# Performance work log

Measured on AMD Instinct MI355X. Metric: run time of the kernel, lower is better.

Reference implementation:

```python
import jax, jax.numpy as jnp
import numpy as np

N, E, IN, ED, HID, B, K = 50000, 800000, 128, 64, 256, 128, 1000


def setup_inputs() -> dict:
    key = jax.random.key(0)
    ks = jax.random.split(key, 16)

    def lin(k, fi, fo):
        k1, k2 = jax.random.split(k)
        s = 1.0 / np.sqrt(fi)
        return (jax.random.uniform(k1, (fi, fo), jnp.float32, -s, s),
                jax.random.uniform(k2, (fo,), jnp.float32, -s, s))

    We, be = lin(ks[0], ED, IN)        # GINEConv edge projection edge_dim -> in_channels
    W1, b1 = lin(ks[1], IN, HID)       # GINE nn layer 1
    W2, b2 = lin(ks[2], HID, HID)      # GINE nn layer 2
    Wg1, bg1 = lin(ks[3], HID, 128)    # gate_nn layer 1
    Wg2, bg2 = lin(ks[4], 128, 1)      # gate_nn layer 2
    Wh, bh = lin(ks[5], HID, K)        # head

    x = jax.random.normal(ks[6], (N, IN), jnp.float32)
    edge_index = jax.random.randint(ks[7], (2, E), 0, N, jnp.int64)
    edge_attr = jax.random.normal(ks[8], (E, ED), jnp.float32)
    batch = jnp.sort(jax.random.randint(ks[9], (N,), 0, B, jnp.int64))

    return {"x": x, "edge_index": edge_index, "edge_attr": edge_attr, "batch": batch,
            "We": We, "be": be, "W1": W1, "b1": b1, "W2": W2, "b2": b2,
            "Wg1": Wg1, "bg1": bg1, "Wg2": Wg2, "bg2": bg2, "Wh": Wh, "bh": bh}


def reference(x, edge_index, edge_attr, batch, We, be, W1, b1, W2, b2,
              Wg1, bg1, Wg2, bg2, Wh, bh):
    src, dst = edge_index[0], edge_index[1]
    # GINEConv message: ReLU(x_j + Lin(edge_attr)), scatter-add to dst (eps=0)
    e = edge_attr @ We + be                      # [E, IN]
    m = jax.nn.relu(x[src] + e)                  # [E, IN]
    agg = jax.ops.segment_sum(m, dst, num_segments=N)  # [N, IN]
    h = x + agg                                  # (1+eps)*x + agg, eps=0
    h = jax.nn.relu(h @ W1 + b1) @ W2 + b2       # [N, HID]
    # GlobalAttention: segment softmax of gate over graphs, weighted sum
    gate = jax.nn.relu(h @ Wg1 + bg1) @ Wg2 + bg2            # [N, 1]
    gmax = jax.ops.segment_max(gate, batch, num_segments=B)  # [B, 1]
    a = jnp.exp(gate - gmax[batch])
    denom = jax.ops.segment_sum(a, batch, num_segments=B)    # [B, 1]
    attn = a / denom[batch]
    pooled = jax.ops.segment_sum(attn * h, batch, num_segments=B)  # [B, HID]
    logits = pooled @ Wh + bh                    # [B, K]
    return (logits, pooled)
```

## Files before the change

### kernel.cpp

```cpp
#include <hip/hip_runtime.h>
#include <stdint.h>

#define NN    50000
#define EE    800000
#define IN_C  128
#define ED_C  64
#define HID_C 256
#define BB    128
#define KK    1000
#define G1_C  128
#define NV    50176


typedef __attribute__((ext_vector_type(8))) short bfrag;
typedef __attribute__((ext_vector_type(4))) float f4acc;

__device__ __forceinline__ unsigned short f2bs(float f){
  unsigned u = __float_as_uint(f);
  return (unsigned short)((u + 0x7fffu + ((u >> 16) & 1u)) >> 16);
}
__device__ __forceinline__ float bs2f(unsigned short s){
  return __uint_as_float(((unsigned)s) << 16);
}

__device__ __forceinline__ void atomicMaxFloat(float* addr, float val){
  int old = __float_as_int(*addr);
  while (__int_as_float(old) < val){
    int assumed = old;
    old = atomicCAS((int*)addr, assumed, __float_as_int(val));
    if (old == assumed) break;
  }
}

__global__ __launch_bounds__(256) void k_prep(
    const float* __restrict__ We, const float* __restrict__ W1,
    const float* __restrict__ W2, const float* __restrict__ Wg1,
    unsigned short* __restrict__ Wet, unsigned short* __restrict__ W1t,
    unsigned short* __restrict__ W2t, unsigned short* __restrict__ Wg1t)
{
  int i = blockIdx.x * 256 + threadIdx.x;
  if (i < 128 * 64){ int c = i >> 6, k = i & 63;  Wet[i]  = f2bs(We[k * 128 + c]); }
  if (i < 256 * 128){ int n = i >> 7, k = i & 127; W1t[i]  = f2bs(W1[k * 256 + n]); }
  if (i < 256 * 256){ int n = i >> 8, k = i & 255; W2t[i]  = f2bs(W2[k * 256 + n]); }
  if (i < 128 * 256){ int n = i >> 8, k = i & 255; Wg1t[i] = f2bs(Wg1[k * 128 + n]); }
}

__global__ __launch_bounds__(256) void k_init(float* __restrict__ agg,
                                              int* __restrict__ cnt,
                                              int* __restrict__ fill,
                                              int* __restrict__ aux,
                                              float* __restrict__ gmax,
                                              float* __restrict__ denom,
                                              float* __restrict__ pooled){
  size_t i = (size_t)blockIdx.x * 256 + threadIdx.x;
  if (i < (size_t)NN * IN_C) agg[i] = 0.f;
  if (i < NV){ cnt[i] = 0; fill[i] = 0; }
  if (i < 256) aux[i] = 0;
  if (i < BB){ gmax[i] = -1e30f; denom[i] = 0.f; }
  if (i < BB * HID_C) pooled[i] = 0.f;
}

__global__ __launch_bounds__(256) void k_hist(const int* __restrict__ ei,
                                              int* __restrict__ cnt){
  int e = blockIdx.x * 256 + threadIdx.x;
  if (e < EE) atomicAdd(&cnt[ei[EE + e]], 1);
}

__global__ __launch_bounds__(256) void k_scan1(const int* __restrict__ cnt,
                                               int* __restrict__ off,
                                               int* __restrict__ aux){
  __shared__ int s[256];
  int t = threadIdx.x, i = blockIdx.x * 256 + t;
  int val = cnt[i];
  s[t] = val; __syncthreads();
#pragma unroll
  for (int o = 1; o < 256; o <<= 1){
    int v = (t >= o) ? s[t - o] : 0;
    __syncthreads();
    s[t] += v;
    __syncthreads();
  }
  off[i] = s[t] - val;
  if (t == 255) aux[blockIdx.x] = s[255];
}

__global__ __launch_bounds__(256) void k_scan2(int* __restrict__ aux){
  __shared__ int s[256];
  int t = threadIdx.x;
  int val = aux[t];
  s[t] = val; __syncthreads();
#pragma unroll
  for (int o = 1; o < 256; o <<= 1){
    int v = (t >= o) ? s[t - o] : 0;
    __syncthreads();
    s[t] += v;
    __syncthreads();
  }
  aux[t] = s[t] - val;
}

__global__ __launch_bounds__(256) void k_scan3(int* __restrict__ off,
                                               const int* __restrict__ aux){
  int i = blockIdx.x * 256 + threadIdx.x;
  off[i] += aux[blockIdx.x];
}

__global__ __launch_bounds__(256) void k_scatter(const int* __restrict__ ei,
                                                 const int* __restrict__ off,
                                                 int* __restrict__ fill,
                                                 uint4* __restrict__ sorted){
  int e = blockIdx.x * 256 + threadIdx.x;
  if (e < EE){
    int s = ei[e], d = ei[EE + e];
    int pos = off[d] + atomicAdd(&fill[d], 1);
    sorted[pos] = make_uint4((unsigned)e, (unsigned)s, (unsigned)d, 0u);
  }
}

__global__ __launch_bounds__(256) void k_edge2(
    const float* __restrict__ x, const uint4* __restrict__ sorted,
    const float* __restrict__ edge_attr,
    const unsigned short* __restrict__ Wet, const float* __restrict__ be,
    float* __restrict__ agg)
{
  __shared__ float msgS[128 * 130];
  __shared__ uint4 sE[128];
  __shared__ float bridgeS[128];
  unsigned short* eaS = (unsigned short*)msgS;

  const int tid = threadIdx.x;
  const int e0 = blockIdx.x * 128;
  if (tid < 128) sE[tid] = sorted[e0 + tid];
  __syncthreads();
#pragma unroll
  for (int t = 0; t < 8; ++t){
    int f4 = t * 256 + tid;
    int er = f4 >> 4;
    int kk = (f4 & 15) * 4;
    int eid = (int)sE[er].x;
    const float4 v = *(const float4*)(edge_attr + (size_t)eid * ED_C + kk);
    unsigned p0 = (unsigned)f2bs(v.x) | ((unsigned)f2bs(v.y) << 16);
    unsigned p1 = (unsigned)f2bs(v.z) | ((unsigned)f2bs(v.w) << 16);
    *(uint2*)&eaS[er * 72 + kk] = make_uint2(p0, p1);
  }
  __syncthreads();

  const int lane = tid & 63, wv = tid >> 6;
  const int q = lane >> 4, l15 = lane & 15;

  f4acc acc[2][8];
  const f4acc zz = {0.f, 0.f, 0.f, 0.f};
#pragma unroll
  for (int mt = 0; mt < 2; ++mt)
#pragma unroll
    for (int nt = 0; nt < 8; ++nt) acc[mt][nt] = zz;

#pragma unroll
  for (int ks = 0; ks < 2; ++ks){
    bfrag a[2], b[8];
#pragma unroll
    for (int mt = 0; mt < 2; ++mt){
      int m = wv * 32 + mt * 16 + l15;
      a[mt] = *(const bfrag*)&eaS[m * 72 + ks * 32 + q * 8];
    }
#pragma unroll
    for (int nt = 0; nt < 8; ++nt){
      int c = nt * 16 + l15;
      b[nt] = *(const bfrag*)(Wet + c * ED_C + ks * 32 + q * 8);
    }
#pragma unroll
    for (int mt = 0; mt < 2; ++mt)
#pragma unroll
      for (int nt = 0; nt < 8; ++nt)
        acc[mt][nt] = __builtin_amdgcn_mfma_f32_16x16x32_bf16(a[mt], b[nt], acc[mt][nt], 0, 0, 0);
  }

  float bev[8];
#pragma unroll
  for (int nt = 0; nt < 8; ++nt) bev[nt] = be[nt * 16 + l15];

  __syncthreads();

#pragma unroll
  for (int mt = 0; mt < 2; ++mt){
    const int g = wv * 32 + mt * 16 + q * 4;
    int sr[4];
#pragma unroll
    for (int r = 0; r < 4; ++r) sr[r] = (int)sE[g + r].y;
#pragma unroll
    for (int nt = 0; nt < 8; ++nt){
      int c = nt * 16 + l15;
#pragma unroll
      for (int r = 0; r < 4; ++r){
        float v = acc[mt][nt][r] + bev[nt] + x[(size_t)sr[r] * IN_C + c];
        v = v > 0.f ? v : 0.f;
        msgS[(g + r) * 130 + c] = v;
      }
    }
  }
  __syncthreads();

  const int col = tid & 127;
  const int h = tid >> 7;
  const int rbeg = h * 64, rend = rbeg + 64;
  const bool bridged = ((int)sE[63].z == (int)sE[64].z);

  int cur = (int)sE[rbeg].z;
  int runstart = rbeg;
  float run = 0.f;
  float firstSum = 0.f; int firstDst = cur;
  bool firstPending = (h == 1);

  for (int r = rbeg; r < rend; ++r){
    int d = (int)sE[r].z;
    if (d != cur){
      if (firstPending){
        firstSum = run; firstDst = cur; firstPending = false;
      } else {
        if (h == 0 && runstart == 0)
          atomicAdd(&agg[(size_t)cur * IN_C + col], run);
        else
          agg[(size_t)cur * IN_C + col] = run;
      }
      run = 0.f; cur = d; runstart = r;
    }
    run += msgS[r * 130 + col];
  }

  if (h == 0){
    if (bridged){
      bridgeS[col] = run;
    } else {
      if (runstart == 0) atomicAdd(&agg[(size_t)cur * IN_C + col], run);
      else               agg[(size_t)cur * IN_C + col] = run;
    }
  }
  __syncthreads();
  if (h == 1){
    if (firstPending){
      float s = run + (bridged ? bridgeS[col] : 0.f);
      atomicAdd(&agg[(size_t)cur * IN_C + col], s);
    } else {
      float s = firstSum + (bridged ? bridgeS[col] : 0.f);
      bool touches0 = bridged && ((int)sE[0].z == firstDst);
      if (touches0) atomicAdd(&agg[(size_t)firstDst * IN_C + col], s);
      else          agg[(size_t)firstDst * IN_C + col] = s;
      atomicAdd(&agg[(size_t)cur * IN_C + col], run);
    }
  }
}

__global__ __launch_bounds__(256) void k_h0(const float* __restrict__ agg,
                                            const float* __restrict__ x,
                                            unsigned short* __restrict__ h0b){
  int i = blockIdx.x * 256 + threadIdx.x;
  if (i < NN * IN_C) h0b[i] = f2bs(agg[i] + x[i]);
}

template<int K, bool RELU, bool OF32, bool OB16>
__global__ __launch_bounds__(256) void k_gemm(
    const unsigned short* __restrict__ A, const unsigned short* __restrict__ Wt,
    const float* __restrict__ bias, float* __restrict__ outf,
    unsigned short* __restrict__ outb, int M, int Ntot)
{
  __shared__ unsigned short aS[64 * 40];
  __shared__ unsigned short bS[128 * 40];
  const int tid = threadIdx.x;
  const int lane = tid & 63, wv = tid >> 6;
  const int wi = wv >> 1, wj = wv & 1;
  const int q = lane >> 4, l15 = lane & 15;
  const int mb0 = blockIdx.x * 64;
  const int nb0 = blockIdx.y * 128;
  const int arow = tid >> 2, achk = tid & 3;

  f4acc acc[2][4];
  const f4acc zz = {0.f, 0.f, 0.f, 0.f};
#pragma unroll
  for (int mt = 0; mt < 2; ++mt)
#pragma unroll
    for (int nt = 0; nt < 4; ++nt) acc[mt][nt] = zz;

  for (int ks = 0; ks < K / 32; ++ks){
    {
      int m = mb0 + arow; if (m >= M) m = M - 1;
      const uint4 v = *(const uint4*)(A + (size_t)m * K + ks * 32 + achk * 8);
      *(uint4*)&aS[arow * 40 + achk * 8] = v;
    }
#pragma unroll
    for (int i = 0; i < 2; ++i){
      int idx = i * 256 + tid;
      int row = idx >> 2, chk = idx & 3;
      const uint4 v = *(const uint4*)(Wt + (size_t)(nb0 + row) * K + ks * 32 + chk * 8);
      *(uint4*)&bS[row * 40 + chk * 8] = v;
    }
    __syncthreads();
    bfrag a[2], b[4];
#pragma unroll
    for (int mt = 0; mt < 2; ++mt)
      a[mt] = *(const bfrag*)&aS[(wi * 32 + mt * 16 + l15) * 40 + q * 8];
#pragma unroll
    for (int nt = 0; nt < 4; ++nt)
      b[nt] = *(const bfrag*)&bS[(wj * 64 + nt * 16 + l15) * 40 + q * 8];
#pragma unroll
    for (int mt = 0; mt < 2; ++mt)
#pragma unroll
      for (int nt = 0; nt < 4; ++nt)
        acc[mt][nt] = __builtin_amdgcn_mfma_f32_16x16x32_bf16(a[mt], b[nt], acc[mt][nt], 0, 0, 0);
    __syncthreads();
  }

  const int mb = mb0 + wi * 32;
  const int nb = nb0 + wj * 64;
#pragma unroll
  for (int nt = 0; nt < 4; ++nt){
    int c = nb + nt * 16 + l15;
    float bv = bias[c];
#pragma unroll
    for (int mt = 0; mt < 2; ++mt){
#pragma unroll
      for (int r = 0; r < 4; ++r){
        int m = mb + mt * 16 + q * 4 + r;
        if (m < M){
          float v = acc[mt][nt][r] + bv;
          if (RELU) v = v > 0.f ? v : 0.f;
          if (OF32) outf[(size_t)m * Ntot + c] = v;
          if (OB16) outb[(size_t)m * Ntot + c] = f2bs(v);
        }
      }
    }
  }
}

__global__ __launch_bounds__(256) void k_gate2(const float* __restrict__ g1,
                                               const float* __restrict__ Wg2,
                                               const float* __restrict__ bg2,
                                               float* __restrict__ gate, int nrows){
  const int lane = threadIdx.x & 63, wv = threadIdx.x >> 6;
  const float2 w2 = *(const float2*)(Wg2 + lane * 2);
  const float bg = bg2[0];
  for (int r = blockIdx.x * 4 + wv; r < nrows; r += gridDim.x * 4){
    const float2 a2 = *(const float2*)(g1 + (size_t)r * G1_C + lane * 2);
    float p = a2.x * w2.x + a2.y * w2.y;
#pragma unroll
    for (int off = 32; off > 0; off >>= 1) p += __shfl_down(p, off);
    if (lane == 0) gate[r] = p + bg;
  }
}

__global__ __launch_bounds__(256) void k_gmax(const float* __restrict__ gate,
                                              const int* __restrict__ batch,
                                              float* __restrict__ gmax, int nrows){
  __shared__ float red[256];
  const int tid = threadIdx.x;
  const int n0 = blockIdx.x * 256;
  const int n = n0 + tid;
  const int nlast = (n0 + 255 < nrows) ? n0 + 255 : nrows - 1;
  const int bmin = batch[n0], bmax = batch[nlast];
  float val = -3e38f; int b = bmax;
  if (n < nrows){ b = batch[n]; val = gate[n]; }
  for (int bb = bmin; bb <= bmax; ++bb){
    red[tid] = (b == bb) ? val : -3e38f;
    __syncthreads();
    for (int s = 128; s > 0; s >>= 1){
      if (tid < s) red[tid] = fmaxf(red[tid], red[tid + s]);
      __syncthreads();
    }
    if (tid == 0 && red[0] > -1e37f) atomicMaxFloat(&gmax[bb], red[0]);
    __syncthreads();
  }
}

__global__ __launch_bounds__(256) void k_expsum(const float* __restrict__ gate,
                                                const int* __restrict__ batch,
                                                const float* __restrict__ gmax,
                                                float* __restrict__ aexp,
                                                float* __restrict__ denom, int nrows){
  __shared__ float red[256];
  const int tid = threadIdx.x;
  const int n0 = blockIdx.x * 256;
  const int n = n0 + tid;
  const int nlast = (n0 + 255 < nrows) ? n0 + 255 : nrows - 1;
  const int bmin = batch[n0], bmax = batch[nlast];
  float val = 0.f; int b = bmax;
  if (n < nrows){
    b = batch[n];
    val = expf(gate[n] - gmax[b]);
    aexp[n] = val;
  }
  for (int bb = bmin; bb <= bmax; ++bb){
    red[tid] = (b == bb) ? val : 0.f;
    __syncthreads();
    for (int s = 128; s > 0; s >>= 1){
      if (tid < s) red[tid] += red[tid + s];
      __syncthreads();
    }
    if (tid == 0 && red[0] != 0.f) atomicAdd(&denom[bb], red[0]);
    __syncthreads();
  }
}

__global__ __launch_bounds__(256) void k_pool(const unsigned short* __restrict__ h2b,
                                              const float* __restrict__ aexp,
                                              const float* __restrict__ denom,
                                              const int* __restrict__ batch,
                                              float* __restrict__ pooled, int nrows){
  const int c = threadIdx.x;
  const int n0 = blockIdx.x * 256;
  int n1 = n0 + 256; if (n1 > nrows) n1 = nrows;
  float acc = 0.f;
  int curb = batch[n0];
  for (int n = n0; n < n1; ++n){
    int b = batch[n];
    if (b != curb){
      atomicAdd(&pooled[(size_t)curb * HID_C + c], acc);
      acc = 0.f; curb = b;
    }
    float wgt = aexp[n] / denom[b];
    acc = fmaf(wgt, bs2f(h2b[(size_t)n * HID_C + c]), acc);
  }
  atomicAdd(&pooled[(size_t)curb * HID_C + c], acc);
}

__global__ __launch_bounds__(256) void k_head(const float* __restrict__ pooled,
                                              const float* __restrict__ Wh,
                                              const float* __restrict__ bh,
                                              float* __restrict__ out_logits,
                                              float* __restrict__ out_pooled){
  __shared__ float p[HID_C];
  const int b = blockIdx.x, t = threadIdx.x;
  float pv = pooled[(size_t)b * HID_C + t];
  p[t] = pv;
  out_pooled[(size_t)b * HID_C + t] = pv;
  __syncthreads();
  for (int c = t; c < KK; c += 256){
    float acc = bh[c];
#pragma unroll 8
    for (int k = 0; k < HID_C; ++k)
      acc = fmaf(p[k], Wh[k * KK + c], acc);
    out_logits[(size_t)b * KK + c] = acc;
  }
}

extern "C" void kernel_launch(void* const* d_in, const int* in_sizes, int n_in,
                              void* d_out, int out_size, void* d_ws, size_t ws_size,
                              hipStream_t stream) {
  const float* x   = (const float*)d_in[0];
  const int*   ei  = (const int*)d_in[1];
  const float* ea  = (const float*)d_in[2];
  const int*   batch = (const int*)d_in[3];
  const float* We  = (const float*)d_in[4];
  const float* be  = (const float*)d_in[5];
  const float* W1  = (const float*)d_in[6];
  const float* b1  = (const float*)d_in[7];
  const float* W2  = (const float*)d_in[8];
  const float* b2  = (const float*)d_in[9];
  const float* Wg1 = (const float*)d_in[10];
  const float* bg1 = (const float*)d_in[11];
  const float* Wg2 = (const float*)d_in[12];
  const float* bg2 = (const float*)d_in[13];
  const float* Wh  = (const float*)d_in[14];
  const float* bh  = (const float*)d_in[15];

  float* out_logits = (float*)d_out;
  float* out_pooled = out_logits + (size_t)BB * KK;

  float* agg    = (float*)d_ws;
  float* gate   = agg   + (size_t)NN * IN_C;
  float* aexp   = gate  + NN;
  float* gmax   = aexp  + NN;
  float* denom  = gmax  + BB;
  float* pooled = denom + BB;
  float* fend   = pooled + (size_t)BB * HID_C;
  unsigned short* h0b  = (unsigned short*)fend;
  unsigned short* h1b  = h0b + (size_t)NN * IN_C;
  unsigned short* h2b  = h1b + (size_t)NN * HID_C;
  unsigned short* Wet  = h2b + (size_t)NN * HID_C;
  unsigned short* W1t  = Wet + 128 * 64;
  unsigned short* W2t  = W1t + 256 * 128;
  unsigned short* Wg1t = W2t + 256 * 256;
  float* g1f = agg;
  uint4* sorted = (uint4*)h1b;
  int* cnt  = (int*)(sorted + EE);
  int* off  = cnt + NV;
  int* fill = off + NV;
  int* aux  = fill + NV;

  k_prep<<<256, 256, 0, stream>>>(We, W1, W2, Wg1, Wet, W1t, W2t, Wg1t);
  k_init<<<(NN * IN_C + 255) / 256, 256, 0, stream>>>(agg, cnt, fill, aux, gmax, denom, pooled);
  k_hist   <<<(EE + 255) / 256, 256, 0, stream>>>(ei, cnt);
  k_scan1  <<<NV / 256, 256, 0, stream>>>(cnt, off, aux);
  k_scan2  <<<1, 256, 0, stream>>>(aux);
  k_scan3  <<<NV / 256, 256, 0, stream>>>(off, aux);
  k_scatter<<<(EE + 255) / 256, 256, 0, stream>>>(ei, off, fill, sorted);
  k_edge2<<<EE / 128, 256, 0, stream>>>(x, sorted, ea, Wet, be, agg);
  k_h0<<<(NN * IN_C + 255) / 256, 256, 0, stream>>>(agg, x, h0b);
  k_gemm<128, true,  false, true ><<<dim3(782, 2), 256, 0, stream>>>(h0b, W1t, b1, (float*)0, h1b, NN, HID_C);
  k_gemm<256, false, false, true ><<<dim3(782, 2), 256, 0, stream>>>(h1b, W2t, b2, (float*)0, h2b, NN, HID_C);
  k_gemm<256, true,  true,  false><<<dim3(782, 1), 256, 0, stream>>>(h2b, Wg1t, bg1, g1f, (unsigned short*)0, NN, G1_C);
  k_gate2<<<3125, 256, 0, stream>>>(g1f, Wg2, bg2, gate, NN);
  k_gmax  <<<(NN + 255) / 256, 256, 0, stream>>>(gate, batch, gmax, NN);
  k_expsum<<<(NN + 255) / 256, 256, 0, stream>>>(gate, batch, gmax, aexp, denom, NN);
  k_pool  <<<(NN + 255) / 256, 256, 0, stream>>>(h2b, aexp, denom, batch, pooled, NN);
  k_head<<<BB, 256, 0, stream>>>(pooled, Wh, bh, out_logits, out_pooled);
}
```

Baseline: 750.5 us.

## Prefetch x rows as float4 and segment-reduce edge messages by precomputed runs

The kernel now issues coalesced float4 loads of each edge's source row of x at kernel start, so the latency overlaps the edge-attr staging and MFMA work. This replaces the per-element scalar gathers that ran after the matmul. Run boundaries of destination nodes are found with a ballot/popcount prefix and stored in shared memory. The two half-blocks then reduce alternating runs, replacing the serial bridged two-half scan. It also pads the shared row stride to 132 and requests two blocks per CU, at the cost of 64 registers per thread for the x prefetch and possible spilling or reduced occupancy.

```diff
diff --git a/kernel.cpp b/kernel.cpp
--- a/kernel.cpp
+++ b/kernel.cpp
@@ -117,21 +117,37 @@
   }
 }
 
-__global__ __launch_bounds__(256) void k_edge2(
+__global__ __launch_bounds__(256, 2) void k_edge2(
     const float* __restrict__ x, const uint4* __restrict__ sorted,
     const float* __restrict__ edge_attr,
     const unsigned short* __restrict__ Wet, const float* __restrict__ be,
     float* __restrict__ agg)
 {
-  __shared__ float msgS[128 * 130];
+  __shared__ float msgS[128 * 132];
   __shared__ uint4 sE[128];
-  __shared__ float bridgeS[128];
+  __shared__ unsigned long long maskS[2];
+  __shared__ int runStart[132];
+  __shared__ int nRunsS;
   unsigned short* eaS = (unsigned short*)msgS;
 
   const int tid = threadIdx.x;
   const int e0 = blockIdx.x * 128;
   if (tid < 128) sE[tid] = sorted[e0 + tid];
   __syncthreads();
+
+  const int xrow = tid >> 1;
+  const int xc0 = (tid & 1) * 64;
+  const float* xptr = x + (size_t)((int)sE[xrow].y) * IN_C + xc0;
+  float4 xr[16];
+#pragma unroll
+  for (int j = 0; j < 16; ++j) xr[j] = *(const float4*)(xptr + j * 4);
+
+  if (tid < 128){
+    bool flag = (tid == 0) || ((int)sE[tid].z != (int)sE[tid - 1].z);
+    unsigned long long m = __ballot(flag);
+    if ((tid & 63) == 0) maskS[tid >> 6] = m;
+  }
+
 #pragma unroll
   for (int t = 0; t < 8; ++t){
     int f4 = t * 256 + tid;
@@ -145,6 +161,18 @@
   }
   __syncthreads();
 
+  if (tid < 128){
+    int lane = tid & 63, wvi = tid >> 6;
+    unsigned long long mw = maskS[wvi];
+    int pre = __popcll(mw & ((1ull << lane) - 1ull)) + (wvi ? __popcll(maskS[0]) : 0);
+    if ((mw >> lane) & 1ull) runStart[pre] = tid;
+    if (tid == 0){
+      int nr = __popcll(maskS[0]) + __popcll(maskS[1]);
+      nRunsS = nr;
+      runStart[nr] = 128;
+    }
+  }
+
   const int lane = tid & 63, wv = tid >> 6;
   const int q = lane >> 4, l15 = lane & 15;
 
@@ -184,68 +212,43 @@
 #pragma unroll
   for (int mt = 0; mt < 2; ++mt){
     const int g = wv * 32 + mt * 16 + q * 4;
-    int sr[4];
-#pragma unroll
-    for (int r = 0; r < 4; ++r) sr[r] = (int)sE[g + r].y;
 #pragma unroll
     for (int nt = 0; nt < 8; ++nt){
       int c = nt * 16 + l15;
 #pragma unroll
-      for (int r = 0; r < 4; ++r){
-        float v = acc[mt][nt][r] + bev[nt] + x[(size_t)sr[r] * IN_C + c];
-        v = v > 0.f ? v : 0.f;
-        msgS[(g + r) * 130 + c] = v;
-      }
+      for (int r = 0; r < 4; ++r)
+        msgS[(g + r) * 132 + c] = acc[mt][nt][r] + bev[nt];
     }
   }
   __syncthreads();
 
-  const int col = tid & 127;
-  const int h = tid >> 7;
-  const int rbeg = h * 64, rend = rbeg + 64;
-  const bool bridged = ((int)sE[63].z == (int)sE[64].z);
-
-  int cur = (int)sE[rbeg].z;
-  int runstart = rbeg;
-  float run = 0.f;
-  float firstSum = 0.f; int firstDst = cur;
-  bool firstPending = (h == 1);
-
-  for (int r = rbeg; r < rend; ++r){
-    int d = (int)sE[r].z;
-    if (d != cur){
-      if (firstPending){
-        firstSum = run; firstDst = cur; firstPending = false;
-      } else {
-        if (h == 0 && runstart == 0)
-          atomicAdd(&agg[(size_t)cur * IN_C + col], run);
-        else
-          agg[(size_t)cur * IN_C + col] = run;
-      }
-      run = 0.f; cur = d; runstart = r;
-    }
-    run += msgS[r * 130 + col];
-  }
-
-  if (h == 0){
-    if (bridged){
-      bridgeS[col] = run;
-    } else {
-      if (runstart == 0) atomicAdd(&agg[(size_t)cur * IN_C + col], run);
-      else               agg[(size_t)cur * IN_C + col] = run;
+  {
+    float* mr = &msgS[xrow * 132 + xc0];
+#pragma unroll
+    for (int j = 0; j < 16; ++j){
+      float4 w = *(float4*)(mr + j * 4);
+      const float4 v = xr[j];
+      w.x = fmaxf(w.x + v.x, 0.f);
+      w.y = fmaxf(w.y + v.y, 0.f);
+      w.z = fmaxf(w.z + v.z, 0.f);
+      w.w = fmaxf(w.w + v.w, 0.f);
+      *(float4*)(mr + j * 4) = w;
     }
   }
   __syncthreads();
-  if (h == 1){
-    if (firstPending){
-      float s = run + (bridged ? bridgeS[col] : 0.f);
-      atomicAdd(&agg[(size_t)cur * IN_C + col], s);
-    } else {
-      float s = firstSum + (bridged ? bridgeS[col] : 0.f);
-      bool touches0 = bridged && ((int)sE[0].z == firstDst);
-      if (touches0) atomicAdd(&agg[(size_t)firstDst * IN_C + col], s);
-      else          agg[(size_t)firstDst * IN_C + col] = s;
-      atomicAdd(&agg[(size_t)cur * IN_C + col], run);
+
+  {
+    const int col = tid & 127;
+    const int h = tid >> 7;
+    const int nR = nRunsS;
+    for (int i = h; i < nR; i += 2){
+      int s = runStart[i], e = runStart[i + 1];
+      int dst = (int)sE[s].z;
+      float run = 0.f;
+      for (int r = s; r < e; ++r) run += msgS[r * 132 + col];
+      size_t a = (size_t)dst * IN_C + col;
+      if (s == 0 || e == 128) atomicAdd(&agg[a], run);
+      else                    agg[a] = run;
     }
   }
 }
```

Result: no change. 749.9 us (-0.1%).
